# Performance work log

Hardware: AMD Instinct MI355X
Metric: run time of the kernel (lower is better)

The kernel has to match this reference:

```python
import jax, jax.numpy as jnp
import numpy as np
from jax import lax

B, T, D_IN, H, L = 256, 160, 40, 768, 3
SCALE = 0.05

def setup_inputs() -> dict:
    key = jax.random.key(0)
    ks = jax.random.split(key, 1 + 3 * L)
    inp = {"x": jax.random.normal(ks[0], (B, T, D_IN), dtype=jnp.float32)}
    in_dims = [D_IN, H, H]
    for l in range(L):
        inp[f"Wi{l}"] = jax.random.normal(ks[1 + 3 * l], (in_dims[l], 4 * H), dtype=jnp.float32) * SCALE
        inp[f"Wh{l}"] = jax.random.normal(ks[2 + 3 * l], (H, 4 * H), dtype=jnp.float32) * SCALE
        inp[f"b{l}"] = jnp.zeros((4 * H,), dtype=jnp.float32)
    return inp

def _lstm_layer(x, Wi, Wh, b):
    # x: [B, T, D]; returns [B, T, H]
    batch = x.shape[0]
    h_dim = Wh.shape[0]
    # Precompute input projections for all timesteps (big GEMM, compute-friendly)
    xw = jnp.einsum('btd,dh->bth', x, Wi) + b  # [B, T, 4H]
    c0 = jnp.zeros((batch, h_dim), dtype=x.dtype)
    h0 = jnp.zeros((batch, h_dim), dtype=x.dtype)

    def step(carry, xw_t):
        c, h = carry
        z = xw_t + h @ Wh  # [B, 4H]
        i, f, g, o = jnp.split(z, 4, axis=-1)  # flax LSTMCell gate order
        i = jax.nn.sigmoid(i)
        f = jax.nn.sigmoid(f)
        g = jnp.tanh(g)
        o = jax.nn.sigmoid(o)
        c_new = f * c + i * g
        h_new = o * jnp.tanh(c_new)
        return (c_new, h_new), h_new

    _, ys = lax.scan(step, (c0, h0), jnp.swapaxes(xw, 0, 1))  # ys: [T, B, H]
    return jnp.swapaxes(ys, 0, 1)

def reference(x, Wi0, Wh0, b0, Wi1, Wh1, b1, Wi2, Wh2, b2):
    h = _lstm_layer(x, Wi0, Wh0, b0)
    h = _lstm_layer(h, Wi1, Wh1, b1)
    h = _lstm_layer(h, Wi2, Wh2, b2)
    # frame_aggregation_mean = True -> mean over time
    return jnp.mean(h, axis=1)
```

## Files before the change

### kernel.cpp

```cpp
#include <hip/hip_runtime.h>
#include <stdint.h>

#define B_   256
#define T_   160
#define DIN_ 40
#define H_   768
#define NG_  3072
#define KP0_ 1024
#define KP12_ 1536
#define XC_  48
#define RS_  16
#define FR_  64
#define BH_  ((size_t)B_ * H_)

typedef _Float16 f16;
typedef _Float16 half8 __attribute__((ext_vector_type(8)));
typedef float f32x4 __attribute__((ext_vector_type(4)));

#define AS1C(p) ((const __attribute__((address_space(1))) uint32_t*)(p))
#define AS3(p)  ((__attribute__((address_space(3))) uint32_t*)(p))

struct Params {
  const f16* wt0; const f16* wt1; const f16* wt2;
  const float* bq; const f16* x16;
  f16* hs0; f16* hs1;
  f16* ring;
  const f16* zpad; unsigned* cnt; unsigned* flgW; unsigned* claim; float* out;
};

__device__ __forceinline__ float sigmoid_f(float x) { return 1.f / (1.f + __expf(-x)); }
__device__ __forceinline__ float tanh_f(float x) {
  x = fminf(15.f, fmaxf(-15.f, x));
  float e = __expf(2.f * x);
  return (e - 1.f) / (e + 1.f);
}

__global__ void conv_w(const float* __restrict__ Wi, const float* __restrict__ Wh,
                       int in_dim, int hoff, int Kp, f16* __restrict__ dst) {
  __shared__ f16 tile[64][66];
  const int k0 = blockIdx.x * 64;
  const int by = blockIdx.y;
  const int g = by / 12, j0 = (by % 12) * 64;
  const int tid = threadIdx.x;
  #pragma unroll
  for (int it = 0; it < 16; ++it) {
    int idx = it * 256 + tid;
    int jj = idx & 63;
    int kk = idx >> 6;
    int k = k0 + kk;
    int oc = g * H_ + j0 + jj;
    float v = 0.f;
    if (k < in_dim) v = Wi[(size_t)k * NG_ + oc];
    else if (k >= hoff && k < hoff + H_) v = Wh[(size_t)(k - hoff) * NG_ + oc];
    tile[kk][jj] = (f16)v;
  }
  __syncthreads();
  #pragma unroll
  for (int it = 0; it < 16; ++it) {
    int idx = it * 256 + tid;
    int kk = idx & 63;
    int jj = idx >> 6;
    int np = 4 * (j0 + jj) + g;
    dst[(size_t)np * Kp + k0 + kk] = tile[kk][jj];
  }
}

__global__ void conv_b(const float* __restrict__ b0, const float* __restrict__ b1,
                       const float* __restrict__ b2, float* __restrict__ bq) {
  int id = blockIdx.x * 256 + threadIdx.x;
  if (id < 3 * NG_) {
    int l = id / NG_, np = id % NG_;
    int j = np >> 2, g = np & 3;
    const float* s = (l == 0) ? b0 : (l == 1 ? b1 : b2);
    bq[id] = s[g * H_ + j];
  }
}

__global__ void conv_x(const float* __restrict__ x, f16* __restrict__ x16) {
  int id = blockIdx.x * 256 + threadIdx.x;
  if (id >= T_ * B_ * XC_) return;
  int k = id % XC_;
  int b = (id / XC_) % B_;
  int t = id / (XC_ * B_);
  float v = (k < DIN_) ? x[(size_t)b * (T_ * DIN_) + t * DIN_ + k] : 0.f;
  x16[id] = (f16)v;
}

template<int L>
__device__ __forceinline__ void run_layer(
    const f16* __restrict__ WT, const f16* __restrict__ hin, f16* __restrict__ hown,
    f16* __restrict__ hring,
    const float* __restrict__ bql, const f16* __restrict__ zpad, float* __restrict__ out,
    unsigned* flg, unsigned* flgW, unsigned& iter, f16* Abuf, float* zred, float* bqs,
    int tid, int lane, int w, int kw, int cw, int btile, int ntile, int n0) {
  constexpr int KP  = (L == 0) ? KP0_ : KP12_;
  constexpr int KQ  = KP / 4;
  constexpr int NKT = KQ / 32;
  constexpr int CH  = (L == 0) ? 128 : 96;

  if (tid < 96) bqs[tid] = bql[tid];

  half8 breg[3 * NKT];
  #pragma unroll
  for (int ct = 0; ct < 3; ++ct) {
    #pragma unroll
    for (int kt = 0; kt < NKT; ++kt) {
      int col = n0 + cw * 48 + ct * 16 + (lane & 15);
      int k = kw * KQ + kt * 32 + (lane >> 4) * 8;
      breg[ct * NKT + kt] = *(const half8*)(WT + (size_t)col * KP + k);
    }
  }

  auto stage_hin = [&](int slot) {
    #pragma unroll
    for (int i = 0; i < 24; ++i) {
      int cb = (w - 6) * 1536 + i * 64;
      int idx = cb + lane;
      int row = idx / 96;
      int c = idx - row * 96;
      int cg = c ^ (row & 7);
      int b = btile * 32 + row;
      const f16* src = hin + ((size_t)slot * B_ + b) * H_ + cg * 8;
      __builtin_amdgcn_global_load_lds(AS1C(src), AS3(Abuf + (size_t)cb * 8), 16, 0, 0);
    }
  };
  if (L > 0 && tid >= 384) stage_hin(1);

  const int id = tid;
  const int grow = id / 12, gjp = id - grow * 12;
  const int gb = btile * 32 + grow;
  const int ghc0 = ntile * 24 + 2 * gjp;
  float c0 = 0.f, c1 = 0.f, oa0 = 0.f, oa1 = 0.f;

  for (int t = 0; t < T_; ++t) {
    const int rslot = t & (RS_ - 1);
    if (L == 0) {
      #pragma unroll
      for (int i = 0; i < 8; ++i) {
        int cb = w * 512 + i * 64;
        int idx = cb + lane;
        int row = idx >> 7;
        int c = idx & 127;
        int cg = c ^ (row & 7);
        int b = btile * 32 + row;
        const f16* src;
        if (cg < 6)        src = hin + ((size_t)t * B_ + b) * XC_ + cg * 8;
        else if (cg < 102) src = hring + ((size_t)rslot * B_ + b) * H_ + (cg - 6) * 8;
        else               src = zpad;
        __builtin_amdgcn_global_load_lds(AS1C(src), AS3(Abuf + (size_t)cb * 8), 16, 0, 0);
      }
    } else if (w >= 4) {
      #pragma unroll
      for (int i = 0; i < 12; ++i) {
        int cb = (w - 4) * 768 + i * 64;
        int idx = cb + lane;
        int row = idx / 96;
        int c = idx - row * 96;
        int cg = c ^ (row & 7);
        int b = btile * 32 + row;
        const f16* src = hring + ((size_t)rslot * B_ + b) * H_ + cg * 8;
        __builtin_amdgcn_global_load_lds(AS1C(src), AS3(Abuf + (size_t)(32 * 768 + cb * 8)), 16, 0, 0);
      }
    }
    asm volatile("s_waitcnt vmcnt(0)" ::: "memory");
    __syncthreads();

    f32x4 acc[2][3] = {};
    const char* Ab = (const char*)(Abuf + (L == 0 ? 0 : (kw >> 1) * 32 * 768));
    const int cbase = (L == 0) ? kw * 32 : (kw & 1) * 48;
    #pragma unroll
    for (int kt = 0; kt < NKT; ++kt) {
      int c = cbase + kt * 4 + (lane >> 4);
      int row0 = (lane & 15);
      half8 a0 = *(const half8*)(Ab + (size_t)row0 * (CH * 16) + (size_t)(c ^ (row0 & 7)) * 16);
      int row1 = 16 + (lane & 15);
      half8 a1 = *(const half8*)(Ab + (size_t)row1 * (CH * 16) + (size_t)(c ^ (row1 & 7)) * 16);
      #pragma unroll
      for (int ct = 0; ct < 3; ++ct) {
        acc[0][ct] = __builtin_amdgcn_mfma_f32_16x16x32_f16(a0, breg[ct * NKT + kt], acc[0][ct], 0, 0, 0);
        acc[1][ct] = __builtin_amdgcn_mfma_f32_16x16x32_f16(a1, breg[ct * NKT + kt], acc[1][ct], 0, 0, 0);
      }
    }

    {
      float* zr = zred + kw * 3072;
      #pragma unroll
      for (int rt = 0; rt < 2; ++rt) {
        #pragma unroll
        for (int ct = 0; ct < 3; ++ct) {
          int row = rt * 16 + (lane >> 4) * 4;
          int col = cw * 48 + ct * 16 + (lane & 15);
          #pragma unroll
          for (int r4 = 0; r4 < 4; ++r4)
            zr[(size_t)(row + r4) * 96 + col] = acc[rt][ct][r4];
        }
      }
    }
    __syncthreads();

    if (tid >= 384) {
      if (L > 0 && t + 1 < T_) stage_hin(t + 2);
    } else {
      const float* z = zred + (size_t)id * 8;
      f32x4 za = *(const f32x4*)(z)        + *(const f32x4*)(z + 3072)
               + *(const f32x4*)(z + 6144) + *(const f32x4*)(z + 9216);
      f32x4 zb = *(const f32x4*)(z + 4)        + *(const f32x4*)(z + 3076)
               + *(const f32x4*)(z + 6148)     + *(const f32x4*)(z + 9220);
      za += *(const f32x4*)(bqs + gjp * 8);
      zb += *(const f32x4*)(bqs + gjp * 8 + 4);
      float i0 = sigmoid_f(za[0]), f0 = sigmoid_f(za[1]), g0 = tanh_f(za[2]), o0 = sigmoid_f(za[3]);
      float i1 = sigmoid_f(zb[0]), f1 = sigmoid_f(zb[1]), g1 = tanh_f(zb[2]), o1 = sigmoid_f(zb[3]);
      float cn0 = f0 * c0 + i0 * g0;
      float cn1 = f1 * c1 + i1 * g1;
      c0 = cn0; c1 = cn1;
      float h0 = o0 * tanh_f(cn0);
      float h1 = o1 * tanh_f(cn1);
      f16 hh0 = (f16)h0, hh1 = (f16)h1;
      unsigned u = ((unsigned)__builtin_bit_cast(uint16_t, hh1) << 16)
                 |  (unsigned)__builtin_bit_cast(uint16_t, hh0);
      unsigned* rp = (unsigned*)(hring + ((size_t)((t + 1) & (RS_ - 1)) * B_ + gb) * H_ + ghc0);
      __hip_atomic_store(rp, u, __ATOMIC_RELAXED, __HIP_MEMORY_SCOPE_WORKGROUP);
      if (L < 2) {
        unsigned* hp = (unsigned*)(hown + ((size_t)(t + 1) * B_ + gb) * H_ + ghc0);
        __hip_atomic_store(hp, u, __ATOMIC_RELAXED, __HIP_MEMORY_SCOPE_WORKGROUP);
      } else {
        oa0 += h0; oa1 += h1;
        if (t == T_ - 1) {
          out[(size_t)gb * H_ + ghc0]     = oa0 * (1.f / T_);
          out[(size_t)gb * H_ + ghc0 + 1] = oa1 * (1.f / T_);
        }
      }
    }

    if (tid < 384) { asm volatile("s_waitcnt vmcnt(0)" ::: "memory"); }
    __syncthreads();
    ++iter;
    if (w == 5) {
      if (lane == 0) {
        __hip_atomic_store(flgW + ((size_t)(iter & (FR_ - 1)) * 32 + ntile) * 32, iter,
                           __ATOMIC_RELAXED, __HIP_MEMORY_SCOPE_WORKGROUP);
        __hip_atomic_store(flg + (size_t)ntile * 32, iter,
                           __ATOMIC_RELAXED, __HIP_MEMORY_SCOPE_AGENT);
      }
      volatile const unsigned* fw =
          flgW + ((size_t)(iter & (FR_ - 1)) * 32 + (lane & 31)) * 32;
      unsigned v = *fw;
      if (__ballot(v >= iter) != ~0ull) {
        unsigned* fp = flg + (size_t)(lane & 31) * 32;
        for (;;) {
          v = __hip_atomic_load(fp, __ATOMIC_RELAXED, __HIP_MEMORY_SCOPE_AGENT);
          if (__ballot(v >= iter) == ~0ull) break;
          __builtin_amdgcn_s_sleep(1);
        }
      }
    }
    __syncthreads();
  }
}

__global__ __launch_bounds__(512, 2) void lstm_main(Params p) {
  __shared__ __align__(16) f16 Abuf[2 * 32 * 768];
  __shared__ __align__(16) float zred[4 * 32 * 96];
  __shared__ __align__(16) float bqs[96];
  __shared__ unsigned claim_s[2];

  const int tid = threadIdx.x;
  const int lane = tid & 63;
  const int w = tid >> 6;
  const int kw = w >> 1, cw = w & 1;

  if (tid == 0) {
    unsigned xcc;
    asm volatile("s_getreg_b32 %0, hwreg(HW_REG_XCC_ID)" : "=s"(xcc));
    xcc &= 7u;
    unsigned slot = __hip_atomic_fetch_add(p.claim + xcc, 1u,
                                           __ATOMIC_RELAXED, __HIP_MEMORY_SCOPE_AGENT);
    claim_s[0] = xcc;
    claim_s[1] = slot & 31u;
  }
  __syncthreads();
  const int btile = (int)claim_s[0];
  const int ntile = (int)claim_s[1];
  unsigned* flg  = p.cnt  + (size_t)btile * 1024;
  unsigned* flgW = p.flgW + (size_t)btile * (FR_ * 32 * 32);
  const int n0 = ntile * 96;
  unsigned iter = 0;

  f16* ring0 = p.ring;
  f16* ring1 = p.ring + (size_t)RS_ * BH_;
  f16* ring2 = p.ring + (size_t)2 * RS_ * BH_;

  run_layer<0>(p.wt0, p.x16, p.hs0, ring0, p.bq + 0 * NG_ + n0, p.zpad, p.out, flg, flgW, iter,
               Abuf, zred, bqs, tid, lane, w, kw, cw, btile, ntile, n0);
  run_layer<1>(p.wt1, p.hs0, p.hs1, ring1, p.bq + 1 * NG_ + n0, p.zpad, p.out, flg, flgW, iter,
               Abuf, zred, bqs, tid, lane, w, kw, cw, btile, ntile, n0);
  run_layer<2>(p.wt2, p.hs1, (f16*)nullptr, ring2, p.bq + 2 * NG_ + n0, p.zpad, p.out, flg, flgW, iter,
               Abuf, zred, bqs, tid, lane, w, kw, cw, btile, ntile, n0);
}

extern "C" void kernel_launch(void* const* d_in, const int* in_sizes, int n_in,
                              void* d_out, int out_size, void* d_ws, size_t ws_size,
                              hipStream_t stream) {
  const float* x   = (const float*)d_in[0];
  const float* Wi0 = (const float*)d_in[1];
  const float* Wh0 = (const float*)d_in[2];
  const float* b0  = (const float*)d_in[3];
  const float* Wi1 = (const float*)d_in[4];
  const float* Wh1 = (const float*)d_in[5];
  const float* b1  = (const float*)d_in[6];
  const float* Wi2 = (const float*)d_in[7];
  const float* Wh2 = (const float*)d_in[8];
  const float* b2  = (const float*)d_in[9];

  char* wsb = (char*)d_ws;
  size_t off = 0;
  auto nxt = [&](size_t sz) { char* p = wsb + off; off += (sz + 255) & ~(size_t)255; return p; };
  f16*      wt0  = (f16*)nxt((size_t)NG_ * KP0_ * 2);
  f16*      wt1  = (f16*)nxt((size_t)NG_ * KP12_ * 2);
  f16*      wt2  = (f16*)nxt((size_t)NG_ * KP12_ * 2);
  float*    bq   = (float*)nxt((size_t)3 * NG_ * 4);
  f16*      x16  = (f16*)nxt((size_t)T_ * B_ * XC_ * 2);
  f16*      hs0  = (f16*)nxt((size_t)(T_ + 1) * BH_ * 2);
  f16*      hs1  = (f16*)nxt((size_t)(T_ + 1) * BH_ * 2);
  f16*      ring = (f16*)nxt((size_t)3 * RS_ * BH_ * 2);
  f16*      zpad = (f16*)nxt(256);
  unsigned* cnt  = (unsigned*)nxt(8 * 1024 * 4);
  unsigned* flgW = (unsigned*)nxt((size_t)8 * FR_ * 32 * 128);
  unsigned* claim= (unsigned*)nxt(256);
  if (off > ws_size) return;

  hipMemsetAsync(ring, 0, BH_ * 2, stream);
  hipMemsetAsync(ring + (size_t)RS_ * BH_, 0, BH_ * 2, stream);
  hipMemsetAsync(ring + (size_t)2 * RS_ * BH_, 0, BH_ * 2, stream);
  hipMemsetAsync(hs0, 0, BH_ * 2, stream);
  hipMemsetAsync(hs1, 0, BH_ * 2, stream);
  hipMemsetAsync((void*)zpad, 0, 256, stream);
  hipMemsetAsync(cnt, 0, 8 * 1024 * 4, stream);
  hipMemsetAsync(flgW, 0, (size_t)8 * FR_ * 32 * 128, stream);
  hipMemsetAsync(claim, 0, 256, stream);

  hipLaunchKernelGGL(conv_w, dim3(KP0_ / 64, 48), dim3(256), 0, stream, Wi0, Wh0, DIN_, XC_, KP0_, wt0);
  hipLaunchKernelGGL(conv_w, dim3(KP12_ / 64, 48), dim3(256), 0, stream, Wi1, Wh1, H_, H_, KP12_, wt1);
  hipLaunchKernelGGL(conv_w, dim3(KP12_ / 64, 48), dim3(256), 0, stream, Wi2, Wh2, H_, H_, KP12_, wt2);
  hipLaunchKernelGGL(conv_b, dim3((3 * NG_ + 255) / 256), dim3(256), 0, stream, b0, b1, b2, bq);
  hipLaunchKernelGGL(conv_x, dim3((T_ * B_ * XC_ + 255) / 256), dim3(256), 0, stream, x, x16);

  Params prm{wt0, wt1, wt2, bq, x16, hs0, hs1, ring, zpad, cnt, flgW, claim, (float*)d_out};
  hipLaunchKernelGGL(lstm_main, dim3(256), dim3(512), 0, stream, prm);
}
```

Baseline: 5.569 ms.

## Replace per-step block barriers with LDS flag handshakes and overlap input-part MFMA

Restructures the per-timestep loop of the persistent LSTM kernel. Most __syncthreads are replaced by fine-grained LDS flag waits between wavefront roles. Waves holding the input-projection K slice now start their MFMA once the prefetched hin tile lands, in parallel with the gate update and the cross-block flag wait. The loop is shifted by one step (gates for t-1, matmul for t) and zred rows are padded to stride 100 to avoid bank conflicts. This aims to cut serialization on the recurrent critical path, but adds spin-wait overhead and risk of ordering bugs in the hand-written handshakes.

```diff
diff --git a/kernel.cpp b/kernel.cpp
--- a/kernel.cpp
+++ b/kernel.cpp
@@ -11,7 +11,14 @@
 #define XC_  48
 #define RS_  16
 #define FR_  64
+#define ZP_  3200
 #define BH_  ((size_t)B_ * H_)
+
+#define FGO 0
+#define FST 1
+#define FGD 9
+#define FMD 15
+#define FPF 19
 
 typedef _Float16 f16;
 typedef _Float16 half8 __attribute__((ext_vector_type(8)));
@@ -33,6 +40,12 @@
   x = fminf(15.f, fmaxf(-15.f, x));
   float e = __expf(2.f * x);
   return (e - 1.f) / (e + 1.f);
+}
+
+__device__ __forceinline__ void spinN(volatile unsigned* s, int i0, int n, unsigned tgt) {
+  for (int i = 0; i < n; ++i) { while (s[i0 + i] < tgt) {} }
+  __builtin_amdgcn_sched_barrier(0);
+  asm volatile("" ::: "memory");
 }
 
 __global__ void conv_w(const float* __restrict__ Wi, const float* __restrict__ Wh,
@@ -88,10 +101,11 @@
 
 template<int L>
 __device__ __forceinline__ void run_layer(
-    const f16* __restrict__ WT, const f16* __restrict__ hin, f16* __restrict__ hown,
-    f16* __restrict__ hring,
+    const f16* __restrict__ WT, const f16* __restrict__ hin, f16* __restrict__ hs_out,
+    f16* __restrict__ ring,
     const float* __restrict__ bql, const f16* __restrict__ zpad, float* __restrict__ out,
     unsigned* flg, unsigned* flgW, unsigned& iter, f16* Abuf, float* zred, float* bqs,
+    volatile unsigned* sflg,
     int tid, int lane, int w, int kw, int cw, int btile, int ntile, int n0) {
   constexpr int KP  = (L == 0) ? KP0_ : KP12_;
   constexpr int KQ  = KP / 4;
@@ -119,55 +133,41 @@
       int row = idx / 96;
       int c = idx - row * 96;
       int cg = c ^ (row & 7);
+      const f16* src = hin + ((size_t)slot * B_ + btile * 32 + row) * H_ + cg * 8;
+      __builtin_amdgcn_global_load_lds(AS1C(src), AS3(Abuf + (size_t)cb * 8), 16, 0, 0);
+    }
+  };
+  auto stage_hown = [&](int t) {
+    const f16* rbase = ring + ((size_t)(t & (RS_ - 1)) * B_) * H_;
+    #pragma unroll
+    for (int i = 0; i < 12; ++i) {
+      int cb = (w - 4) * 768 + i * 64;
+      int idx = cb + lane;
+      int row = idx / 96;
+      int c = idx - row * 96;
+      int cg = c ^ (row & 7);
+      const f16* src = rbase + (size_t)(btile * 32 + row) * H_ + cg * 8;
+      __builtin_amdgcn_global_load_lds(AS1C(src), AS3(Abuf + (size_t)(32 * 768 + cb * 8)), 16, 0, 0);
+    }
+  };
+  auto stage_l0 = [&](int t) {
+    const f16* rbase = ring + ((size_t)(t & (RS_ - 1)) * B_) * H_;
+    #pragma unroll
+    for (int i = 0; i < 8; ++i) {
+      int cb = w * 512 + i * 64;
+      int idx = cb + lane;
+      int row = idx >> 7;
+      int c = idx & 127;
+      int cg = c ^ (row & 7);
       int b = btile * 32 + row;
-      const f16* src = hin + ((size_t)slot * B_ + b) * H_ + cg * 8;
+      const f16* src;
+      if (cg < 6)        src = hin + ((size_t)t * B_ + b) * XC_ + cg * 8;
+      else if (cg < 102) src = rbase + (size_t)b * H_ + (cg - 6) * 8;
+      else               src = zpad;
       __builtin_amdgcn_global_load_lds(AS1C(src), AS3(Abuf + (size_t)cb * 8), 16, 0, 0);
     }
   };
-  if (L > 0 && tid >= 384) stage_hin(1);
-
-  const int id = tid;
-  const int grow = id / 12, gjp = id - grow * 12;
-  const int gb = btile * 32 + grow;
-  const int ghc0 = ntile * 24 + 2 * gjp;
-  float c0 = 0.f, c1 = 0.f, oa0 = 0.f, oa1 = 0.f;
-
-  for (int t = 0; t < T_; ++t) {
-    const int rslot = t & (RS_ - 1);
-    if (L == 0) {
-      #pragma unroll
-      for (int i = 0; i < 8; ++i) {
-        int cb = w * 512 + i * 64;
-        int idx = cb + lane;
-        int row = idx >> 7;
-        int c = idx & 127;
-        int cg = c ^ (row & 7);
-        int b = btile * 32 + row;
-        const f16* src;
-        if (cg < 6)        src = hin + ((size_t)t * B_ + b) * XC_ + cg * 8;
-        else if (cg < 102) src = hring + ((size_t)rslot * B_ + b) * H_ + (cg - 6) * 8;
-        else               src = zpad;
-        __builtin_amdgcn_global_load_lds(AS1C(src), AS3(Abuf + (size_t)cb * 8), 16, 0, 0);
-      }
-    } else if (w >= 4) {
-      #pragma unroll
-      for (int i = 0; i < 12; ++i) {
-        int cb = (w - 4) * 768 + i * 64;
-        int idx = cb + lane;
-        int row = idx / 96;
-        int c = idx - row * 96;
-        int cg = c ^ (row & 7);
-        int b = btile * 32 + row;
-        const f16* src = hring + ((size_t)rslot * B_ + b) * H_ + cg * 8;
-        __builtin_amdgcn_global_load_lds(AS1C(src), AS3(Abuf + (size_t)(32 * 768 + cb * 8)), 16, 0, 0);
-      }
-    }
-    asm volatile("s_waitcnt vmcnt(0)" ::: "memory");
-    __syncthreads();
-
-    f32x4 acc[2][3] = {};
-    const char* Ab = (const char*)(Abuf + (L == 0 ? 0 : (kw >> 1) * 32 * 768));
-    const int cbase = (L == 0) ? kw * 32 : (kw & 1) * 48;
+  auto do_mfma = [&](const char* Ab, int cbase, f32x4 (&acc)[2][3]) {
     #pragma unroll
     for (int kt = 0; kt < NKT; ++kt) {
       int c = cbase + kt * 4 + (lane >> 4);
@@ -181,31 +181,43 @@
         acc[1][ct] = __builtin_amdgcn_mfma_f32_16x16x32_f16(a1, breg[ct * NKT + kt], acc[1][ct], 0, 0, 0);
       }
     }
-
-    {
-      float* zr = zred + kw * 3072;
+  };
+  auto zwrite = [&](int kwp, f32x4 (&acc)[2][3]) {
+    float* zr = zred + (size_t)kwp * ZP_;
+    #pragma unroll
+    for (int rt = 0; rt < 2; ++rt)
       #pragma unroll
-      for (int rt = 0; rt < 2; ++rt) {
+      for (int ct = 0; ct < 3; ++ct)
         #pragma unroll
-        for (int ct = 0; ct < 3; ++ct) {
-          int row = rt * 16 + (lane >> 4) * 4;
-          int col = cw * 48 + ct * 16 + (lane & 15);
-          #pragma unroll
-          for (int r4 = 0; r4 < 4; ++r4)
-            zr[(size_t)(row + r4) * 96 + col] = acc[rt][ct][r4];
-        }
-      }
-    }
-    __syncthreads();
-
-    if (tid >= 384) {
-      if (L > 0 && t + 1 < T_) stage_hin(t + 2);
-    } else {
-      const float* z = zred + (size_t)id * 8;
-      f32x4 za = *(const f32x4*)(z)        + *(const f32x4*)(z + 3072)
-               + *(const f32x4*)(z + 6144) + *(const f32x4*)(z + 9216);
-      f32x4 zb = *(const f32x4*)(z + 4)        + *(const f32x4*)(z + 3076)
-               + *(const f32x4*)(z + 6148)     + *(const f32x4*)(z + 9220);
+        for (int r4 = 0; r4 < 4; ++r4)
+          zr[(size_t)(rt * 16 + (lane >> 4) * 4 + r4) * 100 + cw * 48 + ct * 16 + (lane & 15)]
+            = acc[rt][ct][r4];
+  };
+
+  const int grow = tid / 12, gjp = tid - grow * 12;
+  const int gb = btile * 32 + grow;
+  const int ghc0 = ntile * 24 + 2 * gjp;
+  float c0 = 0.f, c1 = 0.f, oa0 = 0.f, oa1 = 0.f;
+
+  if (L > 0 && w >= 6) stage_hin(1);
+
+  for (int t = 0; t <= T_; ++t) {
+    ++iter;
+    const unsigned it = iter;
+    const bool doG = (t > 0);
+    const bool doM = (t < T_);
+
+    if (L > 0 && w >= 6 && doM) {
+      asm volatile("s_waitcnt vmcnt(0)" ::: "memory");
+      if (lane == 0) sflg[FPF + (w - 6)] = it;
+    }
+
+    if (doG && tid < 384) {
+      const float* z = zred + (size_t)grow * 100 + gjp * 8;
+      f32x4 za = *(const f32x4*)(z)            + *(const f32x4*)(z + ZP_)
+               + *(const f32x4*)(z + 2 * ZP_)  + *(const f32x4*)(z + 3 * ZP_);
+      f32x4 zb = *(const f32x4*)(z + 4)           + *(const f32x4*)(z + 4 + ZP_)
+               + *(const f32x4*)(z + 4 + 2 * ZP_) + *(const f32x4*)(z + 4 + 3 * ZP_);
       za += *(const f32x4*)(bqs + gjp * 8);
       zb += *(const f32x4*)(bqs + gjp * 8 + 4);
       float i0 = sigmoid_f(za[0]), f0 = sigmoid_f(za[1]), g0 = tanh_f(za[2]), o0 = sigmoid_f(za[3]);
@@ -218,57 +230,102 @@
       f16 hh0 = (f16)h0, hh1 = (f16)h1;
       unsigned u = ((unsigned)__builtin_bit_cast(uint16_t, hh1) << 16)
                  |  (unsigned)__builtin_bit_cast(uint16_t, hh0);
-      unsigned* rp = (unsigned*)(hring + ((size_t)((t + 1) & (RS_ - 1)) * B_ + gb) * H_ + ghc0);
+      unsigned* rp = (unsigned*)(ring + ((size_t)(t & (RS_ - 1)) * B_ + gb) * H_ + ghc0);
       __hip_atomic_store(rp, u, __ATOMIC_RELAXED, __HIP_MEMORY_SCOPE_WORKGROUP);
       if (L < 2) {
-        unsigned* hp = (unsigned*)(hown + ((size_t)(t + 1) * B_ + gb) * H_ + ghc0);
+        unsigned* hp = (unsigned*)(hs_out + (size_t)t * BH_ + (size_t)gb * H_ + ghc0);
         __hip_atomic_store(hp, u, __ATOMIC_RELAXED, __HIP_MEMORY_SCOPE_WORKGROUP);
       } else {
         oa0 += h0; oa1 += h1;
-        if (t == T_ - 1) {
+        if (t == T_) {
           out[(size_t)gb * H_ + ghc0]     = oa0 * (1.f / T_);
           out[(size_t)gb * H_ + ghc0 + 1] = oa1 * (1.f / T_);
         }
       }
-    }
-
-    if (tid < 384) { asm volatile("s_waitcnt vmcnt(0)" ::: "memory"); }
-    __syncthreads();
-    ++iter;
-    if (w == 5) {
-      if (lane == 0) {
-        __hip_atomic_store(flgW + ((size_t)(iter & (FR_ - 1)) * 32 + ntile) * 32, iter,
-                           __ATOMIC_RELAXED, __HIP_MEMORY_SCOPE_WORKGROUP);
-        __hip_atomic_store(flg + (size_t)ntile * 32, iter,
-                           __ATOMIC_RELAXED, __HIP_MEMORY_SCOPE_AGENT);
-      }
-      volatile const unsigned* fw =
-          flgW + ((size_t)(iter & (FR_ - 1)) * 32 + (lane & 31)) * 32;
-      unsigned v = *fw;
-      if (__ballot(v >= iter) != ~0ull) {
-        unsigned* fp = flg + (size_t)(lane & 31) * 32;
-        for (;;) {
-          v = __hip_atomic_load(fp, __ATOMIC_RELAXED, __HIP_MEMORY_SCOPE_AGENT);
-          if (__ballot(v >= iter) == ~0ull) break;
-          __builtin_amdgcn_s_sleep(1);
+      asm volatile("s_waitcnt vmcnt(0)" ::: "memory");
+      if (lane == 0) sflg[FGD + w] = it;
+    }
+
+    if (w == 4) {
+      if (doG) {
+        spinN(sflg, FGD, 6, it);
+        if (lane == 0) {
+          __hip_atomic_store(flgW + ((size_t)(it & (FR_ - 1)) * 32 + ntile) * 32, it,
+                             __ATOMIC_RELAXED, __HIP_MEMORY_SCOPE_WORKGROUP);
+          __hip_atomic_store(flg + (size_t)ntile * 32, it,
+                             __ATOMIC_RELAXED, __HIP_MEMORY_SCOPE_AGENT);
+        }
+        if (doM) {
+          volatile const unsigned* fw =
+              (volatile const unsigned*)(flgW + ((size_t)(it & (FR_ - 1)) * 32 + (lane & 31)) * 32);
+          unsigned v = *fw;
+          if (__ballot(v >= it) != ~0ull) {
+            unsigned* fp = flg + (size_t)(lane & 31) * 32;
+            for (;;) {
+              v = __hip_atomic_load(fp, __ATOMIC_RELAXED, __HIP_MEMORY_SCOPE_AGENT);
+              if (__ballot(v >= it) == ~0ull) break;
+              __builtin_amdgcn_s_sleep(1);
+            }
+          }
         }
       }
-    }
-    __syncthreads();
+      if (doM && lane == 0) sflg[FGO] = it;
+    }
+
+    if (doM) {
+      if (L > 0) {
+        if (w < 4) {
+          spinN(sflg, FPF, 2, it);
+          f32x4 acc[2][3] = {};
+          do_mfma((const char*)Abuf, (kw & 1) * 48, acc);
+          asm volatile("s_waitcnt lgkmcnt(0)" ::: "memory");
+          if (lane == 0) sflg[FMD + w] = it;
+          if (doG) spinN(sflg, FGD, 6, it);
+          zwrite(kw, acc);
+        } else {
+          spinN(sflg, FGO, 1, it);
+          stage_hown(t);
+          asm volatile("s_waitcnt vmcnt(0)" ::: "memory");
+          if (lane == 0) sflg[FST + (w - 4)] = it;
+          spinN(sflg, FST, 4, it);
+          f32x4 acc[2][3] = {};
+          do_mfma((const char*)(Abuf + 32 * 768), (kw & 1) * 48, acc);
+          zwrite(kw, acc);
+          if (w >= 6 && t <= T_ - 2) {
+            spinN(sflg, FMD, 4, it);
+            stage_hin(t + 2);
+          }
+        }
+      } else {
+        spinN(sflg, FGO, 1, it);
+        stage_l0(t);
+        asm volatile("s_waitcnt vmcnt(0)" ::: "memory");
+        if (lane == 0) sflg[FST + w] = it;
+        spinN(sflg, FST, 8, it);
+        f32x4 acc[2][3] = {};
+        do_mfma((const char*)Abuf, kw * 32, acc);
+        zwrite(kw, acc);
+      }
+    }
+
+    asm volatile("s_waitcnt lgkmcnt(0)" ::: "memory");
+    __builtin_amdgcn_s_barrier();
   }
 }
 
 __global__ __launch_bounds__(512, 2) void lstm_main(Params p) {
   __shared__ __align__(16) f16 Abuf[2 * 32 * 768];
-  __shared__ __align__(16) float zred[4 * 32 * 96];
+  __shared__ __align__(16) float zred[4 * ZP_];
   __shared__ __align__(16) float bqs[96];
   __shared__ unsigned claim_s[2];
+  __shared__ unsigned sflg_s[32];
 
   const int tid = threadIdx.x;
   const int lane = tid & 63;
   const int w = tid >> 6;
   const int kw = w >> 1, cw = w & 1;
 
+  if (tid < 32) sflg_s[tid] = 0;
   if (tid == 0) {
     unsigned xcc;
     asm volatile("s_getreg_b32 %0, hwreg(HW_REG_XCC_ID)" : "=s"(xcc));
@@ -285,17 +342,18 @@
   unsigned* flgW = p.flgW + (size_t)btile * (FR_ * 32 * 32);
   const int n0 = ntile * 96;
   unsigned iter = 0;
+  volatile unsigned* sflg = (volatile unsigned*)sflg_s;
 
   f16* ring0 = p.ring;
   f16* ring1 = p.ring + (size_t)RS_ * BH_;
   f16* ring2 = p.ring + (size_t)2 * RS_ * BH_;
 
   run_layer<0>(p.wt0, p.x16, p.hs0, ring0, p.bq + 0 * NG_ + n0, p.zpad, p.out, flg, flgW, iter,
-               Abuf, zred, bqs, tid, lane, w, kw, cw, btile, ntile, n0);
+               Abuf, zred, bqs, sflg, tid, lane, w, kw, cw, btile, ntile, n0);
   run_layer<1>(p.wt1, p.hs0, p.hs1, ring1, p.bq + 1 * NG_ + n0, p.zpad, p.out, flg, flgW, iter,
-               Abuf, zred, bqs, tid, lane, w, kw, cw, btile, ntile, n0);
+               Abuf, zred, bqs, sflg, tid, lane, w, kw, cw, btile, ntile, n0);
   run_layer<2>(p.wt2, p.hs1, (f16*)nullptr, ring2, p.bq + 2 * NG_ + n0, p.zpad, p.out, flg, flgW, iter,
-               Abuf, zred, bqs, tid, lane, w, kw, cw, btile, ntile, n0);
+               Abuf, zred, bqs, sflg, tid, lane, w, kw, cw, btile, ntile, n0);
 }
 
 extern "C" void kernel_launch(void* const* d_in, const int* in_sizes, int n_in,
```

New measurement: 7.866 ms. +41.2%, slower.

## Replicate workgroup-scope barrier flags, pad reduction buffer, move hin staging after barrier

Applied to the files above, without the earlier changes.

Each workgroup now writes its step-completion flag into REP_ replicated slots, and the polling wave checks each replica with a ballot before falling back to the agent-scope counter spin. This gives more chances to see every peer's flag through a coherent copy without the slow path. The zred reduction buffer gets a padded row stride (100 floats, 3200 per k-split) to reduce LDS bank conflicts. Prefetching the next layer input moves from the gate phase into the barrier phase on waves 6-7. The cost is more flag stores and workspace, and the extra reads add latency when replicas are not yet visible.

```diff
diff --git a/kernel.cpp b/kernel.cpp
--- a/kernel.cpp
+++ b/kernel.cpp
@@ -11,6 +11,8 @@
 #define XC_  48
 #define RS_  16
 #define FR_  64
+#define REP_ 8
+#define ZP_  3200
 #define BH_  ((size_t)B_ * H_)
 
 typedef _Float16 f16;
@@ -88,8 +90,8 @@
 
 template<int L>
 __device__ __forceinline__ void run_layer(
-    const f16* __restrict__ WT, const f16* __restrict__ hin, f16* __restrict__ hown,
-    f16* __restrict__ hring,
+    const f16* __restrict__ WT, const f16* __restrict__ hin, f16* __restrict__ hs_out,
+    f16* __restrict__ ring,
     const float* __restrict__ bql, const f16* __restrict__ zpad, float* __restrict__ out,
     unsigned* flg, unsigned* flgW, unsigned& iter, f16* Abuf, float* zred, float* bqs,
     int tid, int lane, int w, int kw, int cw, int btile, int ntile, int n0) {
@@ -119,15 +121,13 @@
       int row = idx / 96;
       int c = idx - row * 96;
       int cg = c ^ (row & 7);
-      int b = btile * 32 + row;
-      const f16* src = hin + ((size_t)slot * B_ + b) * H_ + cg * 8;
+      const f16* src = hin + ((size_t)slot * B_ + btile * 32 + row) * H_ + cg * 8;
       __builtin_amdgcn_global_load_lds(AS1C(src), AS3(Abuf + (size_t)cb * 8), 16, 0, 0);
     }
   };
   if (L > 0 && tid >= 384) stage_hin(1);
 
-  const int id = tid;
-  const int grow = id / 12, gjp = id - grow * 12;
+  const int grow = tid / 12, gjp = tid - grow * 12;
   const int gb = btile * 32 + grow;
   const int ghc0 = ntile * 24 + 2 * gjp;
   float c0 = 0.f, c1 = 0.f, oa0 = 0.f, oa1 = 0.f;
@@ -145,7 +145,7 @@
         int b = btile * 32 + row;
         const f16* src;
         if (cg < 6)        src = hin + ((size_t)t * B_ + b) * XC_ + cg * 8;
-        else if (cg < 102) src = hring + ((size_t)rslot * B_ + b) * H_ + (cg - 6) * 8;
+        else if (cg < 102) src = ring + ((size_t)rslot * B_ + b) * H_ + (cg - 6) * 8;
         else               src = zpad;
         __builtin_amdgcn_global_load_lds(AS1C(src), AS3(Abuf + (size_t)cb * 8), 16, 0, 0);
       }
@@ -157,8 +157,7 @@
         int row = idx / 96;
         int c = idx - row * 96;
         int cg = c ^ (row & 7);
-        int b = btile * 32 + row;
-        const f16* src = hring + ((size_t)rslot * B_ + b) * H_ + cg * 8;
+        const f16* src = ring + ((size_t)rslot * B_ + btile * 32 + row) * H_ + cg * 8;
         __builtin_amdgcn_global_load_lds(AS1C(src), AS3(Abuf + (size_t)(32 * 768 + cb * 8)), 16, 0, 0);
       }
     }
@@ -183,7 +182,7 @@
     }
 
     {
-      float* zr = zred + kw * 3072;
+      float* zr = zred + (size_t)kw * ZP_;
       #pragma unroll
       for (int rt = 0; rt < 2; ++rt) {
         #pragma unroll
@@ -192,20 +191,18 @@
           int col = cw * 48 + ct * 16 + (lane & 15);
           #pragma unroll
           for (int r4 = 0; r4 < 4; ++r4)
-            zr[(size_t)(row + r4) * 96 + col] = acc[rt][ct][r4];
+            zr[(size_t)(row + r4) * 100 + col] = acc[rt][ct][r4];
         }
       }
     }
     __syncthreads();
 
-    if (tid >= 384) {
-      if (L > 0 && t + 1 < T_) stage_hin(t + 2);
-    } else {
-      const float* z = zred + (size_t)id * 8;
-      f32x4 za = *(const f32x4*)(z)        + *(const f32x4*)(z + 3072)
-               + *(const f32x4*)(z + 6144) + *(const f32x4*)(z + 9216);
-      f32x4 zb = *(const f32x4*)(z + 4)        + *(const f32x4*)(z + 3076)
-               + *(const f32x4*)(z + 6148)     + *(const f32x4*)(z + 9220);
+    if (tid < 384) {
+      const float* z = zred + (size_t)grow * 100 + (size_t)gjp * 8;
+      f32x4 za = *(const f32x4*)(z)            + *(const f32x4*)(z + ZP_)
+               + *(const f32x4*)(z + 2 * ZP_)  + *(const f32x4*)(z + 3 * ZP_);
+      f32x4 zb = *(const f32x4*)(z + 4)           + *(const f32x4*)(z + 4 + ZP_)
+               + *(const f32x4*)(z + 4 + 2 * ZP_) + *(const f32x4*)(z + 4 + 3 * ZP_);
       za += *(const f32x4*)(bqs + gjp * 8);
       zb += *(const f32x4*)(bqs + gjp * 8 + 4);
       float i0 = sigmoid_f(za[0]), f0 = sigmoid_f(za[1]), g0 = tanh_f(za[2]), o0 = sigmoid_f(za[3]);
@@ -218,10 +215,10 @@
       f16 hh0 = (f16)h0, hh1 = (f16)h1;
       unsigned u = ((unsigned)__builtin_bit_cast(uint16_t, hh1) << 16)
                  |  (unsigned)__builtin_bit_cast(uint16_t, hh0);
-      unsigned* rp = (unsigned*)(hring + ((size_t)((t + 1) & (RS_ - 1)) * B_ + gb) * H_ + ghc0);
+      unsigned* rp = (unsigned*)(ring + ((size_t)((t + 1) & (RS_ - 1)) * B_ + gb) * H_ + ghc0);
       __hip_atomic_store(rp, u, __ATOMIC_RELAXED, __HIP_MEMORY_SCOPE_WORKGROUP);
       if (L < 2) {
-        unsigned* hp = (unsigned*)(hown + ((size_t)(t + 1) * B_ + gb) * H_ + ghc0);
+        unsigned* hp = (unsigned*)(hs_out + (size_t)(t + 1) * BH_ + (size_t)gb * H_ + ghc0);
         __hip_atomic_store(hp, u, __ATOMIC_RELAXED, __HIP_MEMORY_SCOPE_WORKGROUP);
       } else {
         oa0 += h0; oa1 += h1;
@@ -230,29 +227,37 @@
           out[(size_t)gb * H_ + ghc0 + 1] = oa1 * (1.f / T_);
         }
       }
-    }
-
-    if (tid < 384) { asm volatile("s_waitcnt vmcnt(0)" ::: "memory"); }
+      asm volatile("s_waitcnt vmcnt(0)" ::: "memory");
+    }
     __syncthreads();
     ++iter;
     if (w == 5) {
-      if (lane == 0) {
-        __hip_atomic_store(flgW + ((size_t)(iter & (FR_ - 1)) * 32 + ntile) * 32, iter,
+      unsigned* myrow = flgW + ((size_t)(iter & (FR_ - 1)) * 32 + ntile) * REP_ * 32;
+      if (lane < REP_)
+        __hip_atomic_store(myrow + (size_t)lane * 32, iter,
                            __ATOMIC_RELAXED, __HIP_MEMORY_SCOPE_WORKGROUP);
+      if (lane == 0)
         __hip_atomic_store(flg + (size_t)ntile * 32, iter,
                            __ATOMIC_RELAXED, __HIP_MEMORY_SCOPE_AGENT);
-      }
-      volatile const unsigned* fw =
-          flgW + ((size_t)(iter & (FR_ - 1)) * 32 + (lane & 31)) * 32;
-      unsigned v = *fw;
-      if (__ballot(v >= iter) != ~0ull) {
+      asm volatile("s_waitcnt vmcnt(0)" ::: "memory");
+      bool done = false;
+      #pragma unroll
+      for (int r = 0; r < REP_; ++r) {
+        volatile const unsigned* fw =
+            flgW + (((size_t)(iter & (FR_ - 1)) * 32 + (lane & 31)) * REP_ + r) * 32;
+        unsigned v = *fw;
+        if (__ballot(v >= iter) == ~0ull) { done = true; break; }
+      }
+      if (!done) {
         unsigned* fp = flg + (size_t)(lane & 31) * 32;
         for (;;) {
-          v = __hip_atomic_load(fp, __ATOMIC_RELAXED, __HIP_MEMORY_SCOPE_AGENT);
+          unsigned v = __hip_atomic_load(fp, __ATOMIC_RELAXED, __HIP_MEMORY_SCOPE_AGENT);
           if (__ballot(v >= iter) == ~0ull) break;
           __builtin_amdgcn_s_sleep(1);
         }
       }
+    } else if (L > 0 && w >= 6 && t + 1 < T_) {
+      stage_hin(t + 2);
     }
     __syncthreads();
   }
@@ -260,7 +265,7 @@
 
 __global__ __launch_bounds__(512, 2) void lstm_main(Params p) {
   __shared__ __align__(16) f16 Abuf[2 * 32 * 768];
-  __shared__ __align__(16) float zred[4 * 32 * 96];
+  __shared__ __align__(16) float zred[4 * ZP_];
   __shared__ __align__(16) float bqs[96];
   __shared__ unsigned claim_s[2];
 
@@ -282,7 +287,7 @@
   const int btile = (int)claim_s[0];
   const int ntile = (int)claim_s[1];
   unsigned* flg  = p.cnt  + (size_t)btile * 1024;
-  unsigned* flgW = p.flgW + (size_t)btile * (FR_ * 32 * 32);
+  unsigned* flgW = p.flgW + (size_t)btile * ((size_t)FR_ * 32 * REP_ * 32);
   const int n0 = ntile * 96;
   unsigned iter = 0;
 
@@ -315,6 +320,7 @@
   char* wsb = (char*)d_ws;
   size_t off = 0;
   auto nxt = [&](size_t sz) { char* p = wsb + off; off += (sz + 255) & ~(size_t)255; return p; };
+  const size_t flgw_bytes = (size_t)8 * FR_ * 32 * REP_ * 128;
   f16*      wt0  = (f16*)nxt((size_t)NG_ * KP0_ * 2);
   f16*      wt1  = (f16*)nxt((size_t)NG_ * KP12_ * 2);
   f16*      wt2  = (f16*)nxt((size_t)NG_ * KP12_ * 2);
@@ -325,7 +331,7 @@
   f16*      ring = (f16*)nxt((size_t)3 * RS_ * BH_ * 2);
   f16*      zpad = (f16*)nxt(256);
   unsigned* cnt  = (unsigned*)nxt(8 * 1024 * 4);
-  unsigned* flgW = (unsigned*)nxt((size_t)8 * FR_ * 32 * 128);
+  unsigned* flgW = (unsigned*)nxt(flgw_bytes);
   unsigned* claim= (unsigned*)nxt(256);
   if (off > ws_size) return;
 
@@ -336,7 +342,7 @@
   hipMemsetAsync(hs1, 0, BH_ * 2, stream);
   hipMemsetAsync((void*)zpad, 0, 256, stream);
   hipMemsetAsync(cnt, 0, 8 * 1024 * 4, stream);
-  hipMemsetAsync(flgW, 0, (size_t)8 * FR_ * 32 * 128, stream);
+  hipMemsetAsync(flgW, 0, flgw_bytes, stream);
   hipMemsetAsync(claim, 0, 256, stream);
 
   hipLaunchKernelGGL(conv_w, dim3(KP0_ / 64, 48), dim3(256), 0, stream, Wi0, Wh0, DIN_, XC_, KP0_, wt0);
```

Result: slower. 5.722 ms (+2.7%).
